# Performance work log

Hardware: AMD Instinct MI355X
Metric: run time of the kernel (lower is better)

## Reference

```python
import jax, jax.numpy as jnp
import numpy as np

L = 4


def make_coord(h, w):
    # pixel-center coords in [-1,1], shape (h*w, 2), dim order (y, x)
    ys = -1.0 + 1.0 / h + (2.0 / h) * jnp.arange(h, dtype=jnp.float32)
    xs = -1.0 + 1.0 / w + (2.0 / w) * jnp.arange(w, dtype=jnp.float32)
    gy, gx = jnp.meshgrid(ys, xs, indexing='ij')
    return jnp.stack([gy, gx], axis=-1).reshape(-1, 2)


def bilinear_sample(feat, gx, gy):
    # feat: (B,C,H,W); gx,gy in [-1,1], shape (B,N); align_corners=True
    B, C, H, W = feat.shape
    ix = (gx + 1.0) * 0.5 * (W - 1)
    iy = (gy + 1.0) * 0.5 * (H - 1)
    x0f = jnp.floor(ix)
    y0f = jnp.floor(iy)
    x0 = jnp.clip(x0f.astype(jnp.int32), 0, W - 1)
    x1 = jnp.clip(x0 + 1, 0, W - 1)
    y0 = jnp.clip(y0f.astype(jnp.int32), 0, H - 1)
    y1 = jnp.clip(y0 + 1, 0, H - 1)
    wx1 = ix - x0f
    wx0 = 1.0 - wx1
    wy1 = iy - y0f
    wy0 = 1.0 - wy1
    featf = feat.reshape(B, C, H * W)

    def g(yi, xi):
        idx = yi * W + xi  # (B,N)
        return jnp.take_along_axis(featf, idx[:, None, :], axis=2)  # (B,C,N)

    out = (g(y0, x0) * (wy0 * wx0)[:, None, :] + g(y0, x1) * (wy0 * wx1)[:, None, :]
           + g(y1, x0) * (wy1 * wx0)[:, None, :] + g(y1, x1) * (wy1 * wx1)[:, None, :])
    return out.transpose(0, 2, 1)  # (B,N,C)


def pos_enc(x):
    # x: (B,N,2) -> (B,N,4L); per dim: [sin_0..sin_{L-1}, cos_0..cos_{L-1}]
    freq = (2.0 ** jnp.arange(L, dtype=jnp.float32)) * np.pi
    spec = x[..., None] * freq  # (B,N,2,L)
    enc = jnp.concatenate([jnp.sin(spec), jnp.cos(spec)], axis=-1)  # (B,N,2,2L)
    return enc.reshape(*x.shape[:-1], 4 * L)


def mlp(x, w0, b0, w1, b1, w2, b2, w3, b3):
    h = jax.nn.relu(x @ w0 + b0)
    h = jax.nn.relu(h @ w1 + b1)
    h = jax.nn.relu(h @ w2 + b2)
    return h @ w3 + b3


def setup_inputs() -> dict:
    key = jax.random.key(0)
    ks = jax.random.split(key, 8)
    B, C, H, W = 4, 64, 128, 128
    hid, out_dim = 256, 3
    in_dim = C + 2 + 4 * L + 2  # 84
    s = 0.05
    return {
        'inp': jax.random.normal(ks[0], (B, C, H, W), jnp.float32),
        'w0': jax.random.normal(ks[1], (in_dim, hid), jnp.float32) * s,
        'b0': jnp.zeros((hid,), jnp.float32),
        'w1': jax.random.normal(ks[2], (hid, hid), jnp.float32) * s,
        'b1': jnp.zeros((hid,), jnp.float32),
        'w2': jax.random.normal(ks[3], (hid, hid), jnp.float32) * s,
        'b2': jnp.zeros((hid,), jnp.float32),
        'w3': jax.random.normal(ks[4], (hid, out_dim), jnp.float32) * s,
        'b3': jnp.zeros((out_dim,), jnp.float32),
        'scale': 2,
    }


def reference(inp, w0, b0, w1, b1, w2, b2, w3, b3, scale):
    B, C, H, W = inp.shape
    th, tw = int(round(H * scale)), int(round(W * scale))
    N = th * tw
    coord = jnp.broadcast_to(make_coord(th, tw)[None], (B, N, 2))
    # cell = (2/th, 2/tw); rel_cell = cell * (H, W)
    rel_cell = jnp.broadcast_to(
        jnp.array([2.0 / th * H, 2.0 / tw * W], jnp.float32), (B, N, 2))
    # feature-pixel coordinate map, appended as extra channels so one gather serves both
    fc = make_coord(H, W).reshape(H, W, 2).transpose(2, 0, 1)  # (2,H,W)
    aug = jnp.concatenate([inp, jnp.broadcast_to(fc[None], (B, 2, H, W))], axis=1)

    pe = pos_enc(coord)  # same for all 4 ensemble branches
    hw_scale = jnp.array([H, W], jnp.float32)
    rx, ry = 1.0 / H, 1.0 / W
    eps = 1e-6

    preds, areas = [], []
    for vx in (-1, 1):
        for vy in (-1, 1):
            c0 = jnp.clip(coord[..., 0] + vx * rx + eps, -1 + 1e-6, 1 - 1e-6)
            c1 = jnp.clip(coord[..., 1] + vy * ry + eps, -1 + 1e-6, 1 - 1e-6)
            # grid_sample uses (x, y) = flipped coord -> gx=c1, gy=c0
            q = bilinear_sample(aug, c1, c0)  # (B,N,C+2)
            q_feat, q_coord = q[..., :C], q[..., C:]
            rel = (coord - q_coord) * hw_scale  # (B,N,2)
            x = jnp.concatenate([q_feat, rel, pe, rel_cell], axis=-1)
            preds.append(mlp(x, w0, b0, w1, b1, w2, b2, w3, b3))
            areas.append(jnp.abs(rel[..., 0] * rel[..., 1]) + 1e-9)

    areas = [areas[3], areas[2], areas[1], areas[0]]  # diagonal swap
    tot = areas[0] + areas[1] + areas[2] + areas[3]
    ret = sum(p * (a / tot)[..., None] for p, a in zip(preds, areas))  # (B,N,out)
    return ret.reshape(B, th, tw, -1).transpose(0, 3, 1, 2)  # (B,out,th,tw)
```

## Files before the change

### kernel.cpp

```cpp
#include <hip/hip_runtime.h>
#include <math.h>

#define NB 4
#define NH 128
#define NW 128
#define TH 256
#define TW 256
#define AST 264
#define K0 96
#define MROWS 256
#define PIXB 64

typedef _Float16 f16;
typedef f16  f16x8 __attribute__((ext_vector_type(8)));
typedef f16  f16x4v __attribute__((ext_vector_type(4)));
typedef float f32x4 __attribute__((ext_vector_type(4)));

#define OFF_W1 24576
#define OFF_W2 (OFF_W1 + 65536)
#define OFF_W3 (OFF_W2 + 65536)
#define WS_W_ELEMS (OFF_W3 + 4096)
#define FT_ELEMS (NB * NH * NW * 64)

__global__ void cvt_weights(const float* __restrict__ w0, const float* __restrict__ w1,
                            const float* __restrict__ w2, const float* __restrict__ w3,
                            f16* __restrict__ ws) {
  const int i = blockIdx.x * 256 + threadIdx.x;
  if (i < 24576) {
    const int n = i / 96, k = i - n * 96;
    ws[i] = (k < 84) ? (f16)w0[k * 256 + n] : (f16)0.f;
  } else if (i < OFF_W2) {
    const int j = i - OFF_W1; const int n = j >> 8, k = j & 255;
    ws[i] = (f16)w1[k * 256 + n];
  } else if (i < OFF_W3) {
    const int j = i - OFF_W2; const int n = j >> 8, k = j & 255;
    ws[i] = (f16)w2[k * 256 + n];
  } else if (i < WS_W_ELEMS) {
    const int j = i - OFF_W3; const int n = j >> 8, k = j & 255;
    ws[i] = (n < 3) ? (f16)w3[k * 3 + n] : (f16)0.f;
  }
}

__global__ void transpose_feat(const float* __restrict__ feat, f16* __restrict__ ft) {
  __shared__ f16 tile[64][66];
  const int bid = blockIdx.x;
  const int xt = bid & 1, y = (bid >> 1) & 127, b = bid >> 8;
  const int x0 = xt * 64;
  {
    const int c4 = threadIdx.x >> 6, x = threadIdx.x & 63;
#pragma unroll
    for (int co = 0; co < 16; ++co) {
      const int c = co * 4 + c4;
      tile[x][c] = (f16)feat[((size_t)(b * 64 + c) * NH + y) * NW + x0 + x];
    }
  }
  __syncthreads();
  {
    const int x4 = threadIdx.x >> 6, c = threadIdx.x & 63;
#pragma unroll
    for (int xo = 0; xo < 16; ++xo) {
      const int x = xo * 4 + x4;
      ft[((size_t)(b * NH + y) * NW + x0 + x) * 64 + c] = tile[x][c];
    }
  }
}

template<int K>
__device__ __forceinline__ void dense_layer(const f16* __restrict__ Wt,
                                            const float* __restrict__ bias,
                                            f16* act, int wm, int wn, int l) {
  constexpr int NK = K / 32;
  const int nl = l & 15, kq = l >> 4;
  const f16* Abase = Wt + (size_t)(wn * 64 + nl) * K + kq * 8;
  const f16* Bbase = act + (wm * 128 + nl) * AST + kq * 8;

  f32x4 acc[4][8];
#pragma unroll
  for (int nf = 0; nf < 4; ++nf) {
    const float4 b4 = *(const float4*)(bias + wn * 64 + nf * 16 + kq * 4);
    f32x4 a; a[0] = b4.x; a[1] = b4.y; a[2] = b4.z; a[3] = b4.w;
#pragma unroll
    for (int mf = 0; mf < 8; ++mf) acc[nf][mf] = a;
  }

  f16x8 A0[4], A1[4], B[8];
#pragma unroll
  for (int nf = 0; nf < 4; ++nf) A0[nf] = *(const f16x8*)(Abase + nf * 16 * K);

#pragma unroll
  for (int ks = 0; ks < NK; ++ks) {
    f16x8* cur = (ks & 1) ? A1 : A0;
    f16x8* nxt = (ks & 1) ? A0 : A1;
    if (ks + 1 < NK) {
#pragma unroll
      for (int nf = 0; nf < 4; ++nf)
        nxt[nf] = *(const f16x8*)(Abase + (ks + 1) * 32 + nf * 16 * K);
    }
#pragma unroll
    for (int mf = 0; mf < 8; ++mf)
      B[mf] = *(const f16x8*)(Bbase + ks * 32 + mf * 16 * AST);
#pragma unroll
    for (int nf = 0; nf < 4; ++nf)
#pragma unroll
      for (int mf = 0; mf < 8; ++mf)
        acc[nf][mf] = __builtin_amdgcn_mfma_f32_16x16x32_f16(cur[nf], B[mf], acc[nf][mf], 0, 0, 0);
  }

  __syncthreads();

#pragma unroll
  for (int nf = 0; nf < 4; ++nf)
#pragma unroll
    for (int mf = 0; mf < 8; ++mf) {
      f16x4v o;
      o[0] = (f16)fmaxf(acc[nf][mf][0], 0.f);
      o[1] = (f16)fmaxf(acc[nf][mf][1], 0.f);
      o[2] = (f16)fmaxf(acc[nf][mf][2], 0.f);
      o[3] = (f16)fmaxf(acc[nf][mf][3], 0.f);
      *(f16x4v*)(act + (wm * 128 + mf * 16 + nl) * AST + wn * 64 + nf * 16 + kq * 4) = o;
    }
}

template<bool USE_FT>
__global__ __launch_bounds__(512, 2) void inr2d_mfma(
    const float* __restrict__ feat, const f16* __restrict__ ft,
    const float* __restrict__ b0, const float* __restrict__ b1,
    const float* __restrict__ b2, const float* __restrict__ b3,
    const f16* __restrict__ ws, float* __restrict__ out)
{
  __shared__ f16 act[MROWS][AST];
  __shared__ float area_s[MROWS];
  __shared__ float pred_s[MROWS][4];

  const int t = threadIdx.x;
  const int blk = ((blockIdx.x & 7) << 9) | (blockIdx.x >> 3);

  {
    const int r = t >> 1, sub = t & 1;
    const int pix = r >> 2, e = r & 3;
    const int gp = blk * PIXB + pix;
    const int b = gp >> 16, rem = gp & 65535;
    const int oy = rem >> 8, ox = rem & 255;

    const float cy = (2.0f * oy + 1.0f) / (float)TH - 1.0f;
    const float cx = (2.0f * ox + 1.0f) / (float)TW - 1.0f;
    const float vx = (e & 2) ? 1.0f : -1.0f;
    const float vy = (e & 1) ? 1.0f : -1.0f;
    const float rr = 1.0f / (float)NH;

    float c0 = fminf(fmaxf(cy + vx * rr + 1e-6f, -1.0f + 1e-6f), 1.0f - 1e-6f);
    float c1 = fminf(fmaxf(cx + vy * rr + 1e-6f, -1.0f + 1e-6f), 1.0f - 1e-6f);

    const float ix = (c1 + 1.0f) * 0.5f * (float)(NW - 1);
    const float iy = (c0 + 1.0f) * 0.5f * (float)(NH - 1);
    const float x0f = floorf(ix), y0f = floorf(iy);
    int x0 = (int)x0f; x0 = max(0, min(x0, NW - 1));
    int x1 = min(x0 + 1, NW - 1);
    int y0 = (int)y0f; y0 = max(0, min(y0, NH - 1));
    int y1 = min(y0 + 1, NH - 1);
    const float wx1 = ix - x0f, wx0 = 1.0f - wx1;
    const float wy1 = iy - y0f, wy0 = 1.0f - wy1;
    const float w00 = wy0 * wx0, w01 = wy0 * wx1, w10 = wy1 * wx0, w11 = wy1 * wx1;

    if (USE_FT) {
      const f16* fb = ft + (size_t)b * (NH * NW * 64);
      const f16* r00 = fb + (size_t)(y0 * NW + x0) * 64 + sub * 32;
      const f16* r01 = fb + (size_t)(y0 * NW + x1) * 64 + sub * 32;
      const f16* r10 = fb + (size_t)(y1 * NW + x0) * 64 + sub * 32;
      const f16* r11 = fb + (size_t)(y1 * NW + x1) * 64 + sub * 32;
#pragma unroll
      for (int h = 0; h < 4; ++h) {
        const f16x8 a00 = *(const f16x8*)(r00 + h * 8);
        const f16x8 a01 = *(const f16x8*)(r01 + h * 8);
        const f16x8 a10 = *(const f16x8*)(r10 + h * 8);
        const f16x8 a11 = *(const f16x8*)(r11 + h * 8);
#pragma unroll
        for (int i = 0; i < 8; ++i) {
          const float v = w00 * (float)a00[i] + w01 * (float)a01[i] +
                          w10 * (float)a10[i] + w11 * (float)a11[i];
          act[r][sub * 32 + h * 8 + i] = (f16)v;
        }
      }
    } else {
      const float* fb = feat + (size_t)b * 64 * NH * NW;
      const int i00 = y0 * NW + x0, i01 = y0 * NW + x1;
      const int i10 = y1 * NW + x0, i11 = y1 * NW + x1;
#pragma unroll
      for (int i = 0; i < 32; ++i) {
        const int c = sub * 32 + i;
        const float* fc = fb + (size_t)c * (NH * NW);
        const float v = w00 * fc[i00] + w01 * fc[i01] + w10 * fc[i10] + w11 * fc[i11];
        act[r][c] = (f16)v;
      }
    }
    if (sub == 0) {
      const float qy = -1.0f + 1.0f / NH + (2.0f / NH) * (wy0 * (float)y0 + wy1 * (float)y1);
      const float qx = -1.0f + 1.0f / NW + (2.0f / NW) * (wx0 * (float)x0 + wx1 * (float)x1);
      const float rely = (cy - qy) * (float)NH;
      const float relx = (cx - qx) * (float)NW;
      act[r][64] = (f16)rely;
      act[r][65] = (f16)relx;
#pragma unroll
      for (int ll = 0; ll < 4; ++ll) {
        const float f = (float)(1 << ll) * (float)M_PI;
        act[r][66 + ll] = (f16)sinf(cy * f);
        act[r][70 + ll] = (f16)cosf(cy * f);
        act[r][74 + ll] = (f16)sinf(cx * f);
        act[r][78 + ll] = (f16)cosf(cx * f);
      }
      act[r][82] = (f16)1.0f;
      act[r][83] = (f16)1.0f;
#pragma unroll
      for (int z = 84; z < K0; ++z) act[r][z] = (f16)0.f;
      area_s[r] = fabsf(rely * relx) + 1e-9f;
    }
  }
  __syncthreads();

  const int w = t >> 6, l = t & 63;
  const int wm = w >> 2, wn = w & 3;

  dense_layer<K0 >(ws,          b0, &act[0][0], wm, wn, l);
  __syncthreads();
  dense_layer<256>(ws + OFF_W1, b1, &act[0][0], wm, wn, l);
  __syncthreads();
  dense_layer<256>(ws + OFF_W2, b2, &act[0][0], wm, wn, l);
  __syncthreads();

  {
    const int nl = l & 15, kq = l >> 4;
    const f16* Abase = ws + OFF_W3 + nl * 256 + kq * 8;
#pragma unroll
    for (int p = 0; p < 2; ++p) {
      const f16* Bbase = &act[w * 32 + p * 16 + nl][0] + kq * 8;
      f32x4 acc = {0.f, 0.f, 0.f, 0.f};
#pragma unroll
      for (int ks = 0; ks < 8; ++ks) {
        f16x8 a = *(const f16x8*)(Abase + ks * 32);
        f16x8 b = *(const f16x8*)(Bbase + ks * 32);
        acc = __builtin_amdgcn_mfma_f32_16x16x32_f16(a, b, acc, 0, 0, 0);
      }
      if (l < 16) {
        float4 pr;
        pr.x = acc[0] + b3[0]; pr.y = acc[1] + b3[1]; pr.z = acc[2] + b3[2]; pr.w = 0.f;
        *(float4*)(&pred_s[w * 32 + p * 16 + l][0]) = pr;
      }
    }
  }
  __syncthreads();

  if (t < PIXB * 3) {
    const int pix = t / 3, o = t - pix * 3;
    const int gp = blk * PIXB + pix;
    const int b = gp >> 16, rem = gp & 65535;
    const int oy = rem >> 8, ox = rem & 255;
    const int r0 = pix * 4;
    const float a0 = area_s[r0], a1 = area_s[r0 + 1], a2 = area_s[r0 + 2], a3 = area_s[r0 + 3];
    const float tot = a0 + a1 + a2 + a3;
    const float v = pred_s[r0][o] * a3 + pred_s[r0 + 1][o] * a2 +
                    pred_s[r0 + 2][o] * a1 + pred_s[r0 + 3][o] * a0;
    out[(((size_t)b * 3 + o) << 16) + (oy << 8) + ox] = v / tot;
  }
}

extern "C" void kernel_launch(void* const* d_in, const int* in_sizes, int n_in,
                              void* d_out, int out_size, void* d_ws, size_t ws_size,
                              hipStream_t stream) {
  const float* feat = (const float*)d_in[0];
  const float* w0 = (const float*)d_in[1];
  const float* b0 = (const float*)d_in[2];
  const float* w1 = (const float*)d_in[3];
  const float* b1 = (const float*)d_in[4];
  const float* w2 = (const float*)d_in[5];
  const float* b2 = (const float*)d_in[6];
  const float* w3 = (const float*)d_in[7];
  const float* b3 = (const float*)d_in[8];
  float* out = (float*)d_out;
  f16* ws = (f16*)d_ws;

  cvt_weights<<<(WS_W_ELEMS + 255) / 256, 256, 0, stream>>>(w0, w1, w2, w3, ws);

  const int blocks = (NB * TH * TW) / PIXB;
  const bool use_ft = ws_size >= (size_t)(WS_W_ELEMS + FT_ELEMS) * sizeof(f16);
  if (use_ft) {
    f16* ft = ws + WS_W_ELEMS;
    transpose_feat<<<NB * NH * (NW / 64), 256, 0, stream>>>(feat, ft);
    inr2d_mfma<true><<<blocks, 512, 0, stream>>>(feat, ft, b0, b1, b2, b3, ws, out);
  } else {
    inr2d_mfma<false><<<blocks, 512, 0, stream>>>(feat, nullptr, b0, b1, b2, b3, ws, out);
  }
}
```

Baseline: 460.1 us.

## Switch MLP layers to 32x32x16 MFMA with triple-buffered operands and precomputed PE table

Rewrites the dense layer to use 32x32x16 f16 MFMA tiles (2x4 per wave) instead of 16x16x32, which halves the number of fragment loads per FLOP. A/B fragments are now triple-buffered, with loads issued two k-steps ahead. The positional-encoding sin/cos values are precomputed into a lookup table in the weight buffer and read from it on the ft path, removing per-pixel transcendental math. Risks are higher register pressure from the 16-wide accumulators and a larger operand buffer at 2 blocks per CU.

```diff
diff --git a/kernel.cpp b/kernel.cpp
--- a/kernel.cpp
+++ b/kernel.cpp
@@ -15,11 +15,13 @@
 typedef f16  f16x8 __attribute__((ext_vector_type(8)));
 typedef f16  f16x4v __attribute__((ext_vector_type(4)));
 typedef float f32x4 __attribute__((ext_vector_type(4)));
+typedef float f32x16 __attribute__((ext_vector_type(16)));
 
 #define OFF_W1 24576
 #define OFF_W2 (OFF_W1 + 65536)
 #define OFF_W3 (OFF_W2 + 65536)
-#define WS_W_ELEMS (OFF_W3 + 4096)
+#define OFF_PE (OFF_W3 + 4096)
+#define WS_W_ELEMS (OFF_PE + 4096)
 #define FT_ELEMS (NB * NH * NW * 64)
 
 __global__ void cvt_weights(const float* __restrict__ w0, const float* __restrict__ w1,
@@ -35,9 +37,15 @@
   } else if (i < OFF_W3) {
     const int j = i - OFF_W2; const int n = j >> 8, k = j & 255;
     ws[i] = (f16)w2[k * 256 + n];
-  } else if (i < WS_W_ELEMS) {
+  } else if (i < OFF_PE) {
     const int j = i - OFF_W3; const int n = j >> 8, k = j & 255;
     ws[i] = (n < 3) ? (f16)w3[k * 3 + n] : (f16)0.f;
+  } else if (i < WS_W_ELEMS) {
+    const int j = i - OFF_PE;
+    const int o = (j & 2047) >> 3, e = j & 7;
+    const float c = (2.0f * o + 1.0f) / 256.0f - 1.0f;
+    const float f = (float)(1 << (e & 3)) * (float)M_PI;
+    ws[i] = (f16)((e < 4) ? sinf(c * f) : cosf(c * f));
   }
 }
 
@@ -69,56 +77,66 @@
 __device__ __forceinline__ void dense_layer(const f16* __restrict__ Wt,
                                             const float* __restrict__ bias,
                                             f16* act, int wm, int wn, int l) {
-  constexpr int NK = K / 32;
-  const int nl = l & 15, kq = l >> 4;
-  const f16* Abase = Wt + (size_t)(wn * 64 + nl) * K + kq * 8;
-  const f16* Bbase = act + (wm * 128 + nl) * AST + kq * 8;
-
-  f32x4 acc[4][8];
-#pragma unroll
-  for (int nf = 0; nf < 4; ++nf) {
-    const float4 b4 = *(const float4*)(bias + wn * 64 + nf * 16 + kq * 4);
-    f32x4 a; a[0] = b4.x; a[1] = b4.y; a[2] = b4.z; a[3] = b4.w;
-#pragma unroll
-    for (int mf = 0; mf < 8; ++mf) acc[nf][mf] = a;
-  }
-
-  f16x8 A0[4], A1[4], B[8];
-#pragma unroll
-  for (int nf = 0; nf < 4; ++nf) A0[nf] = *(const f16x8*)(Abase + nf * 16 * K);
+  constexpr int NK = K / 16;
+  const int lo = l & 31, hi = l >> 5;
+  const f16* Abase = Wt + (size_t)(wn * 64 + lo) * K + hi * 8;
+  const f16* Bbase = act + (wm * 128 + lo) * AST + hi * 8;
+
+  f32x16 acc[2][4];
+#pragma unroll
+  for (int nt = 0; nt < 2; ++nt) {
+    f32x16 ci;
+#pragma unroll
+    for (int g = 0; g < 4; ++g) {
+      const float4 b4 = *(const float4*)(bias + wn * 64 + nt * 32 + 8 * g + 4 * hi);
+      ci[4 * g + 0] = b4.x; ci[4 * g + 1] = b4.y; ci[4 * g + 2] = b4.z; ci[4 * g + 3] = b4.w;
+    }
+#pragma unroll
+    for (int mt = 0; mt < 4; ++mt) acc[nt][mt] = ci;
+  }
+
+  f16x8 Ab[3][2], Bb[3][4];
+#pragma unroll
+  for (int p = 0; p < 2; ++p) {
+#pragma unroll
+    for (int nt = 0; nt < 2; ++nt) Ab[p][nt] = *(const f16x8*)(Abase + nt * 32 * K + p * 16);
+#pragma unroll
+    for (int mt = 0; mt < 4; ++mt) Bb[p][mt] = *(const f16x8*)(Bbase + mt * 32 * AST + p * 16);
+  }
 
 #pragma unroll
   for (int ks = 0; ks < NK; ++ks) {
-    f16x8* cur = (ks & 1) ? A1 : A0;
-    f16x8* nxt = (ks & 1) ? A0 : A1;
-    if (ks + 1 < NK) {
-#pragma unroll
-      for (int nf = 0; nf < 4; ++nf)
-        nxt[nf] = *(const f16x8*)(Abase + (ks + 1) * 32 + nf * 16 * K);
-    }
-#pragma unroll
-    for (int mf = 0; mf < 8; ++mf)
-      B[mf] = *(const f16x8*)(Bbase + ks * 32 + mf * 16 * AST);
-#pragma unroll
-    for (int nf = 0; nf < 4; ++nf)
-#pragma unroll
-      for (int mf = 0; mf < 8; ++mf)
-        acc[nf][mf] = __builtin_amdgcn_mfma_f32_16x16x32_f16(cur[nf], B[mf], acc[nf][mf], 0, 0, 0);
-  }
-
-  __syncthreads();
-
-#pragma unroll
-  for (int nf = 0; nf < 4; ++nf)
-#pragma unroll
-    for (int mf = 0; mf < 8; ++mf) {
-      f16x4v o;
-      o[0] = (f16)fmaxf(acc[nf][mf][0], 0.f);
-      o[1] = (f16)fmaxf(acc[nf][mf][1], 0.f);
-      o[2] = (f16)fmaxf(acc[nf][mf][2], 0.f);
-      o[3] = (f16)fmaxf(acc[nf][mf][3], 0.f);
-      *(f16x4v*)(act + (wm * 128 + mf * 16 + nl) * AST + wn * 64 + nf * 16 + kq * 4) = o;
-    }
+    if (ks + 2 < NK) {
+      const int d = (ks + 2) % 3;
+#pragma unroll
+      for (int nt = 0; nt < 2; ++nt) Ab[d][nt] = *(const f16x8*)(Abase + nt * 32 * K + (ks + 2) * 16);
+#pragma unroll
+      for (int mt = 0; mt < 4; ++mt) Bb[d][mt] = *(const f16x8*)(Bbase + mt * 32 * AST + (ks + 2) * 16);
+    }
+    const int c = ks % 3;
+#pragma unroll
+    for (int mt = 0; mt < 4; ++mt)
+#pragma unroll
+      for (int nt = 0; nt < 2; ++nt)
+        acc[nt][mt] = __builtin_amdgcn_mfma_f32_32x32x16_f16(Ab[c][nt], Bb[c][mt], acc[nt][mt], 0, 0, 0);
+  }
+
+  __syncthreads();
+
+#pragma unroll
+  for (int nt = 0; nt < 2; ++nt)
+#pragma unroll
+    for (int mt = 0; mt < 4; ++mt)
+#pragma unroll
+      for (int g = 0; g < 4; ++g) {
+        f16x4v o;
+        o[0] = (f16)fmaxf(acc[nt][mt][4 * g + 0], 0.f);
+        o[1] = (f16)fmaxf(acc[nt][mt][4 * g + 1], 0.f);
+        o[2] = (f16)fmaxf(acc[nt][mt][4 * g + 2], 0.f);
+        o[3] = (f16)fmaxf(acc[nt][mt][4 * g + 3], 0.f);
+        *(f16x4v*)(act + (size_t)(wm * 128 + mt * 32 + lo) * AST +
+                   wn * 64 + nt * 32 + 8 * g + 4 * hi) = o;
+      }
 }
 
 template<bool USE_FT>
@@ -200,13 +218,20 @@
       const float relx = (cx - qx) * (float)NW;
       act[r][64] = (f16)rely;
       act[r][65] = (f16)relx;
-#pragma unroll
-      for (int ll = 0; ll < 4; ++ll) {
-        const float f = (float)(1 << ll) * (float)M_PI;
-        act[r][66 + ll] = (f16)sinf(cy * f);
-        act[r][70 + ll] = (f16)cosf(cy * f);
-        act[r][74 + ll] = (f16)sinf(cx * f);
-        act[r][78 + ll] = (f16)cosf(cx * f);
+      if (USE_FT) {
+        const f16* py = ws + OFF_PE + (size_t)oy * 8;
+        const f16* px = ws + OFF_PE + 2048 + (size_t)ox * 8;
+#pragma unroll
+        for (int j = 0; j < 8; ++j) { act[r][66 + j] = py[j]; act[r][74 + j] = px[j]; }
+      } else {
+#pragma unroll
+        for (int ll = 0; ll < 4; ++ll) {
+          const float f = (float)(1 << ll) * (float)M_PI;
+          act[r][66 + ll] = (f16)sinf(cy * f);
+          act[r][70 + ll] = (f16)cosf(cy * f);
+          act[r][74 + ll] = (f16)sinf(cx * f);
+          act[r][78 + ll] = (f16)cosf(cx * f);
+        }
       }
       act[r][82] = (f16)1.0f;
       act[r][83] = (f16)1.0f;
```

Result: faster. 440.7 us (-4.2%).
